# Kernel tuning notes

Hardware: AMD Instinct MI355X
Metric: run time of the kernel (lower is better)

Reference implementation:

```python
import jax, jax.numpy as jnp
import numpy as np
from jax import lax

PRE_NMS_TOPN = 6000
POST_NMS_TOPN = 300
NMS_IOU = 0.7
VARIANCES = np.array([0.1, 0.1, 0.2, 0.2], dtype=np.float32)


def setup_inputs() -> dict:
    key = jax.random.key(0)
    k1, k2, k3, k4 = jax.random.split(key, 4)
    B, FH, FW, K = 32, 128, 128, 9
    A = FH * FW * K  # 147456 total anchors
    rpn_bbox_deltas = jax.random.normal(k1, (B, A, 4), dtype=jnp.float32) * 0.1
    rpn_labels = jax.random.normal(k2, (B, FH, FW, K), dtype=jnp.float32)
    # Anchors in [y1, x1, y2, x2] with y1<y2, x1<x2 on a ~1024px image.
    ctr = jax.random.uniform(k3, (A, 2), dtype=jnp.float32) * 1024.0
    wh = jax.random.uniform(k4, (A, 2), dtype=jnp.float32) * 224.0 + 32.0
    anchors = jnp.concatenate([ctr - 0.5 * wh, ctr + 0.5 * wh], axis=-1)
    return {"rpn_bbox_deltas": rpn_bbox_deltas, "rpn_labels": rpn_labels, "anchors": anchors}


def get_bboxes_from_deltas(anchors, deltas):
    # anchors: [A, 4] (y1,x1,y2,x2); deltas: [B, A, 4] (dy,dx,dh,dw)
    anc_w = anchors[..., 3] - anchors[..., 1]
    anc_h = anchors[..., 2] - anchors[..., 0]
    anc_cx = anchors[..., 1] + 0.5 * anc_w
    anc_cy = anchors[..., 0] + 0.5 * anc_h
    bb_w = jnp.exp(deltas[..., 3]) * anc_w
    bb_h = jnp.exp(deltas[..., 2]) * anc_h
    bb_cx = deltas[..., 1] * anc_w + anc_cx
    bb_cy = deltas[..., 0] * anc_h + anc_cy
    y1 = bb_cy - 0.5 * bb_h
    x1 = bb_cx - 0.5 * bb_w
    y2 = bb_h + y1
    x2 = bb_w + x1
    return jnp.stack([y1, x1, y2, x2], axis=-1)


def nms_per_image(boxes, scores, iou_threshold, num_keep):
    # boxes: [N, 4] sorted by descending score; scores: [N]
    y1, x1, y2, x2 = boxes[:, 0], boxes[:, 1], boxes[:, 2], boxes[:, 3]
    areas = (y2 - y1) * (x2 - x1)

    def step(scores_rem, _):
        idx = jnp.argmax(scores_rem)
        valid = jnp.isfinite(scores_rem[idx])
        b = boxes[idx]
        iy1 = jnp.maximum(b[0], y1)
        ix1 = jnp.maximum(b[1], x1)
        iy2 = jnp.minimum(b[2], y2)
        ix2 = jnp.minimum(b[3], x2)
        inter = jnp.clip(iy2 - iy1, 0.0) * jnp.clip(ix2 - ix1, 0.0)
        b_area = (b[2] - b[0]) * (b[3] - b[1])
        iou = inter / (areas + b_area - inter + 1e-9)
        # IoU(box, itself) == 1 > threshold, so the picked box is also suppressed.
        new_scores = jnp.where(iou > iou_threshold, -jnp.inf, scores_rem)
        return new_scores, (idx, valid)

    _, (keep_idx, valid) = lax.scan(step, scores, None, length=num_keep)
    vf = valid.astype(boxes.dtype)
    keep_boxes = boxes[keep_idx] * vf[:, None]  # zero-pad invalid slots
    keep_scores = scores[keep_idx] * vf
    return keep_boxes, keep_scores


def reference(rpn_bbox_deltas, rpn_labels, anchors):
    A = anchors.shape[0]
    B = rpn_bbox_deltas.shape[0]
    deltas = rpn_bbox_deltas.reshape(B, A, 4) * jnp.asarray(VARIANCES)
    labels = jax.nn.softmax(rpn_labels, axis=-1).reshape(B, A)
    rpn_bboxes = get_bboxes_from_deltas(anchors, deltas)  # [B, A, 4]
    # top-k pre-NMS filter (lax.top_k output is already sorted descending)
    pre_scores, pre_idx = lax.top_k(labels, PRE_NMS_TOPN)  # [B, P]
    pre_boxes = jnp.take_along_axis(rpn_bboxes, pre_idx[..., None], axis=1)  # [B, P, 4]
    nms_fn = lambda b, s: nms_per_image(b, s, NMS_IOU, POST_NMS_TOPN)
    roi_bboxes, roi_scores = jax.vmap(nms_fn)(pre_boxes, pre_scores)
    return roi_bboxes, roi_scores
```

## Files before the change

### kernel.cpp

```cpp
#include <hip/hip_runtime.h>
#include <cstdint>
#include <cstddef>

#pragma clang fp contract(off)

#define KCLS 9
#define PRE_N 6000
#define POST_N 300
#define NMS_IOU_T 0.7f
#define HIST_BLOCK 256
#define CHUNKS_PER_IMG 32
#define NMS_BLOCK 512
#define PICK_BLOCK 256
#define NSEG 4
#define SEG_CAP 4096

__global__ void __launch_bounds__(256)
softmax_hist_kernel(const float* __restrict__ labels,
                    float* __restrict__ scores,
                    unsigned int* __restrict__ ghist,
                    int ngroups, int gpi) {
    __shared__ unsigned int h[2048];
    const int tid = threadIdx.x;
    for (int i = tid; i < 2048; i += 256) h[i] = 0u;
    __syncthreads();
    const int g = blockIdx.x * 256 + tid;
    if (g < ngroups) {
        const float* x = labels + (size_t)g * KCLS;
        float v[KCLS];
        float m = -1e30f;
        #pragma unroll
        for (int k = 0; k < KCLS; ++k) { v[k] = x[k]; m = fmaxf(m, v[k]); }
        float e[KCLS];
        float s = 0.f;
        #pragma unroll
        for (int k = 0; k < KCLS; ++k) { e[k] = expf(v[k] - m); s += e[k]; }
        float* o = scores + (size_t)g * KCLS;
        #pragma unroll
        for (int k = 0; k < KCLS; ++k) {
            float r = e[k] / s;
            o[k] = r;
            atomicAdd(&h[(__float_as_uint(r) >> 21) & 2047u], 1u);
        }
    }
    __syncthreads();
    const int img0 = (blockIdx.x * 256) / gpi;
    unsigned int* gh = ghist + (size_t)img0 * 2048;
    for (int i = tid; i < 2048; i += 256) {
        unsigned int c = h[i];
        if (c) atomicAdd(&gh[i], c);
    }
}

__global__ void hist_kernel(const float* __restrict__ scores,
                            unsigned int* __restrict__ ghist,
                            const unsigned int* __restrict__ state,
                            int A, int shift, int bins, unsigned int pmask) {
    __shared__ unsigned int h[2048];
    const int img = blockIdx.y;
    const int chunk = blockIdx.x;
    const int tid = threadIdx.x;
    for (int i = tid; i < bins; i += HIST_BLOCK) h[i] = 0u;
    __syncthreads();
    unsigned int prefix = pmask ? (state[img * 2 + 0] & pmask) : 0u;
    const int per = A / CHUNKS_PER_IMG;
    const float* sc = scores + (size_t)img * A + (size_t)chunk * per;
    for (int i = tid; i < per; i += HIST_BLOCK) {
        unsigned int v = __float_as_uint(sc[i]);
        if ((v & pmask) == prefix)
            atomicAdd(&h[(v >> shift) & (unsigned)(bins - 1)], 1u);
    }
    __syncthreads();
    unsigned int* gh = ghist + (size_t)img * 2048;
    for (int i = tid; i < bins; i += HIST_BLOCK) {
        unsigned int c = h[i];
        if (c) atomicAdd(&gh[i], c);
    }
}

__global__ void __launch_bounds__(PICK_BLOCK)
pick_kernel(const unsigned int* __restrict__ ghist,
            unsigned int* __restrict__ state,
            int shift, int bins, int first_pass) {
    const int img = blockIdx.x;
    const int t = threadIdx.x;
    const unsigned int* gh = ghist + (size_t)img * 2048;
    __shared__ unsigned int cnt[2048];
    __shared__ unsigned int ssum[PICK_BLOCK];
    const int per = bins / PICK_BLOCK;
    unsigned int my = 0;
    for (int i = 0; i < per; ++i) {
        unsigned int c = gh[t * per + i];
        cnt[t * per + i] = c;
        my += c;
    }
    ssum[t] = my;
    __syncthreads();
    for (int d = 1; d < PICK_BLOCK; d <<= 1) {
        unsigned int v = (t + d < PICK_BLOCK) ? ssum[t + d] : 0u;
        __syncthreads();
        ssum[t] += v;
        __syncthreads();
    }
    unsigned int prefix = first_pass ? 0u : state[img * 2 + 0];
    unsigned int krem = first_pass ? (unsigned)PRE_N : state[img * 2 + 1];
    unsigned int above = ssum[t] - my;
    if (above < krem && ssum[t] >= krem) {
        unsigned int cum = above;
        for (int b = per - 1; b >= 0; --b) {
            unsigned int c = cnt[t * per + b];
            if (cum + c >= krem) {
                state[img * 2 + 0] = prefix | ((unsigned int)(t * per + b) << shift);
                state[img * 2 + 1] = krem - cum;
                break;
            }
            cum += c;
        }
    }
}

#define CE(a, b, u) { if ((v[a] > v[b]) == (u)) { unsigned long long t_ = v[a]; v[a] = v[b]; v[b] = t_; } }
#define REG3(u) { CE(0,4,u) CE(1,5,u) CE(2,6,u) CE(3,7,u) \
                  CE(0,2,u) CE(1,3,u) CE(4,6,u) CE(5,7,u) \
                  CE(0,1,u) CE(2,3,u) CE(4,5,u) CE(6,7,u) }

__global__ void __launch_bounds__(512)
compact_sort_kernel(const float* __restrict__ scores,
                    const unsigned int* __restrict__ state,
                    unsigned long long* __restrict__ pool,
                    unsigned int* __restrict__ counts,
                    int A) {
    __shared__ unsigned long long lin[SEG_CAP];
    __shared__ unsigned int plo[2][SEG_CAP];
    __shared__ unsigned int phi[2][SEG_CAP];
    __shared__ unsigned int cnt;
    const int img = blockIdx.y;
    const int seg = blockIdx.x;
    const int tid = threadIdx.x;
    const int lane = tid & 63;
    const int w = tid >> 6;
    const float* sc = scores + (size_t)img * A;
    const unsigned int T = state[img * 2 + 0];

    if (tid == 0) cnt = 0u;
    for (int i = tid; i < SEG_CAP; i += 512) lin[i] = ~0ull;
    __syncthreads();

    const int ngr = A >> 6;
    const int nj = ngr / NSEG;
    for (int j = w; j < nj; j += 8) {
        int g = seg + j * NSEG;
        int i = (g << 6) + lane;
        unsigned int sv = __float_as_uint(sc[i]);
        bool push = (sv >= T);
        unsigned long long bal = __ballot(push ? 1 : 0);
        if (push) {
            int leader = __ffsll(bal) - 1;
            int rank = __popcll(bal & ((1ull << lane) - 1ull));
            unsigned int base = 0;
            if (lane == leader) base = atomicAdd(&cnt, (unsigned int)__popcll(bal));
            base = (unsigned int)__shfl((int)base, leader);
            unsigned int pos = base + (unsigned int)rank;
            if (pos < SEG_CAP)
                lin[pos] = (((unsigned long long)(~sv)) << 32) | (unsigned long long)(unsigned int)i;
        }
    }
    __syncthreads();

    int n = (int)cnt; if (n > SEG_CAP) n = SEG_CAP;
    int P2 = 512; while (P2 < n) P2 <<= 1;
    const int NT = P2 >> 3;
    const int t = tid;
    const bool act = (t < NT);

    unsigned long long v[8];
    if (act) {
        #pragma unroll
        for (int e = 0; e < 8; ++e) v[e] = lin[(t << 3) + e];
        CE(0,1,true) CE(2,3,false) CE(4,5,true) CE(6,7,false)
        CE(0,2,true) CE(1,3,true) CE(4,6,false) CE(5,7,false)
        CE(0,1,true) CE(2,3,true) CE(4,5,false) CE(6,7,false)
        bool u8 = ((t & 1) == 0);
        REG3(u8)
    }
    int b = 0;
    for (int k = 16; k <= P2; k <<= 1) {
        const bool up = (((t << 3) & k) == 0);
        for (int j = k >> 1; j >= 8; j >>= 1) {
            const int c = j >> 3;
            if (act) {
                #pragma unroll
                for (int e = 0; e < 8; ++e) {
                    int idx = e * NT + t;
                    plo[b][idx] = (unsigned int)v[e];
                    phi[b][idx] = (unsigned int)(v[e] >> 32);
                }
            }
            __syncthreads();
            if (act) {
                const int q = t ^ c;
                const bool keep_min = (up == ((t & c) == 0));
                #pragma unroll
                for (int e = 0; e < 8; ++e) {
                    int idx = e * NT + q;
                    unsigned long long wv = ((unsigned long long)phi[b][idx] << 32)
                                          | (unsigned long long)plo[b][idx];
                    bool less = v[e] < wv;
                    v[e] = (less == keep_min) ? v[e] : wv;
                }
            }
            b ^= 1;
        }
        if (act) { REG3(up) }
    }

    unsigned long long* gp = pool + ((size_t)img * NSEG + seg) * SEG_CAP;
    if (act) {
        #pragma unroll
        for (int e = 0; e < 8; ++e) {
            int r = (t << 3) + e;
            if (r < n) gp[r] = v[e];
        }
    }
    if (tid == 0) counts[img * NSEG + seg] = (unsigned int)n;
}

__global__ void __launch_bounds__(256)
rank_decode_kernel(const unsigned long long* __restrict__ pool,
                   const unsigned int* __restrict__ counts,
                   const float* __restrict__ deltas,
                   const float* __restrict__ anchors,
                   float* __restrict__ pre_boxes,
                   float* __restrict__ pre_scores,
                   int A) {
    __shared__ unsigned long long arr[2 * SEG_CAP];
    const int img = blockIdx.y;
    const int seg = blockIdx.x;
    const int tid = threadIdx.x;

    int c[NSEG], off[NSEG + 1];
    const unsigned long long* gp[NSEG];
    off[0] = 0;
    #pragma unroll
    for (int s = 0; s < NSEG; ++s) {
        int cs = (int)counts[img * NSEG + s];
        if (cs > SEG_CAP) cs = SEG_CAP;
        c[s] = cs;
        off[s + 1] = off[s] + cs;
        gp[s] = pool + ((size_t)img * NSEG + s) * SEG_CAP;
    }
    const int total = off[NSEG];
    const bool inlds = (total <= 2 * SEG_CAP);
    if (inlds) {
        #pragma unroll
        for (int s = 0; s < NSEG; ++s)
            for (int i = tid; i < c[s]; i += 256) arr[off[s] + i] = gp[s][i];
    }
    __syncthreads();

    const int m = c[seg];
    for (int i = tid; i < m; i += 256) {
        unsigned long long key = inlds ? arr[off[seg] + i] : gp[seg][i];
        int pos = i;
        #pragma unroll
        for (int s = 0; s < NSEG; ++s) {
            if (s == seg) continue;
            const unsigned long long* base = inlds ? (arr + off[s]) : gp[s];
            int lo = 0, hi = c[s];
            while (lo < hi) {
                int mid = (lo + hi) >> 1;
                if (base[mid] < key) lo = mid + 1; else hi = mid;
            }
            pos += lo;
        }
        if (pos < PRE_N) {
            unsigned int bidx = (unsigned int)(key & 0xFFFFFFFFull);
            unsigned int sbits = ~((unsigned int)(key >> 32));
            float score = __uint_as_float(sbits);
            float a0 = anchors[(size_t)bidx * 4 + 0];
            float a1 = anchors[(size_t)bidx * 4 + 1];
            float a2 = anchors[(size_t)bidx * 4 + 2];
            float a3 = anchors[(size_t)bidx * 4 + 3];
            const float* dd = deltas + ((size_t)img * A + bidx) * 4;
            float d0 = dd[0] * 0.1f;
            float d1 = dd[1] * 0.1f;
            float d2 = dd[2] * 0.2f;
            float d3 = dd[3] * 0.2f;
            float anc_w = a3 - a1;
            float anc_h = a2 - a0;
            float anc_cx = a1 + 0.5f * anc_w;
            float anc_cy = a0 + 0.5f * anc_h;
            float bb_w = expf(d3) * anc_w;
            float bb_h = expf(d2) * anc_h;
            float bb_cx = d1 * anc_w + anc_cx;
            float bb_cy = d0 * anc_h + anc_cy;
            float y1 = bb_cy - 0.5f * bb_h;
            float x1 = bb_cx - 0.5f * bb_w;
            float y2 = bb_h + y1;
            float x2 = bb_w + x1;
            float* ob = pre_boxes + ((size_t)img * PRE_N + pos) * 4;
            ob[0] = y1; ob[1] = x1; ob[2] = y2; ob[3] = x2;
            pre_scores[(size_t)img * PRE_N + pos] = score;
        }
    }
}

__global__ void __launch_bounds__(NMS_BLOCK)
nms_kernel(const float* __restrict__ pre_boxes,
           const float* __restrict__ pre_scores,
           float* __restrict__ out_boxes,
           float* __restrict__ out_scores) {
    const int img = blockIdx.x;
    const int tid = threadIdx.x;
    const int lane = tid & 63;
    const int grp = tid >> 6;
    const float4* bb4 = (const float4*)(pre_boxes + (size_t)img * PRE_N * 4);

    __shared__ float4 kept[POST_N];
    __shared__ float  kept_area[POST_N];
    __shared__ int    kept_idx[POST_N];
    __shared__ float4 chunkbox[64];
    __shared__ unsigned long long chunk_alive;
    __shared__ int kept_cnt;

    if (tid == 0) kept_cnt = 0;

    const int NCH = (PRE_N + 63) >> 6;

    float4 nb = make_float4(0.f, 0.f, 0.f, 0.f);
    if (grp == 0) nb = bb4[lane];

    for (int c = 0; c < NCH; ++c) {
        const int base = c << 6;
        if (grp == 0) chunkbox[lane] = nb;
        if (tid == 0) {
            int rem = PRE_N - base;
            chunk_alive = (rem >= 64) ? ~0ull : ((1ull << rem) - 1ull);
        }
        __syncthreads();

        if (grp == 0 && c + 1 < NCH) {
            int j = base + 64 + lane;
            nb = (j < PRE_N) ? bb4[j] : make_float4(0.f, 0.f, 0.f, 0.f);
        }

        const int K = kept_cnt;
        float4 mb = chunkbox[lane];
        float marea = (mb.z - mb.x) * (mb.w - mb.y);

        bool sup = false;
        for (int k = grp; k < K; k += 8) {
            float4 pb = kept[k];
            float pa = kept_area[k];
            float iy1 = fmaxf(pb.x, mb.x);
            float ix1 = fmaxf(pb.y, mb.y);
            float iy2 = fminf(pb.z, mb.z);
            float ix2 = fminf(pb.w, mb.w);
            float ih = iy2 - iy1; ih = ih > 0.f ? ih : 0.f;
            float iw = ix2 - ix1; iw = iw > 0.f ? iw : 0.f;
            float inter = ih * iw;
            float den = marea + pa - inter + 1e-9f;
            float hi = 0.7000007f * den;
            float lo = 0.6999993f * den;
            bool s = inter > hi;
            if (inter >= lo && inter <= hi)
                s = (inter / den) > NMS_IOU_T;
            if (s) { sup = true; break; }
        }
        unsigned long long bal = __ballot(sup ? 1 : 0);
        if (lane == 0 && bal) atomicAnd(&chunk_alive, ~bal);
        __syncthreads();

        if (grp == 0) {
            unsigned long long m = chunk_alive;
            int kc = K;
            while (m && kc < POST_N) {
                int i = __ffsll(m) - 1;
                float py1 = __shfl(mb.x, i);
                float px1 = __shfl(mb.y, i);
                float py2 = __shfl(mb.z, i);
                float px2 = __shfl(mb.w, i);
                float pa  = __shfl(marea, i);
                if (lane == i) {
                    kept[kc] = mb;
                    kept_area[kc] = marea;
                    kept_idx[kc] = base + i;
                }
                float iy1 = fmaxf(py1, mb.x);
                float ix1 = fmaxf(px1, mb.y);
                float iy2 = fminf(py2, mb.z);
                float ix2 = fminf(px2, mb.w);
                float ih = iy2 - iy1; ih = ih > 0.f ? ih : 0.f;
                float iw = ix2 - ix1; iw = iw > 0.f ? iw : 0.f;
                float inter = ih * iw;
                float den = marea + pa - inter + 1e-9f;
                float hi = 0.7000007f * den;
                float lo = 0.6999993f * den;
                bool s = inter > hi;
                if (inter >= lo && inter <= hi)
                    s = (inter / den) > NMS_IOU_T;
                unsigned long long sb = __ballot(s ? 1 : 0);
                m &= ~sb;
                m &= ~(1ull << i);
                ++kc;
            }
            if (lane == 0) kept_cnt = kc;
        }
        __syncthreads();
        if (kept_cnt >= POST_N) break;
    }

    const int kc = kept_cnt;
    for (int r = tid; r < kc; r += NMS_BLOCK) {
        float4 bx = kept[r];
        float* ob = out_boxes + ((size_t)img * POST_N + r) * 4;
        ob[0] = bx.x; ob[1] = bx.y; ob[2] = bx.z; ob[3] = bx.w;
        out_scores[(size_t)img * POST_N + r] =
            pre_scores[(size_t)img * PRE_N + kept_idx[r]];
    }
}

extern "C" void kernel_launch(void* const* d_in, const int* in_sizes, int n_in,
                              void* d_out, int out_size, void* d_ws, size_t ws_size,
                              hipStream_t stream) {
    const float* deltas  = (const float*)d_in[0];
    const float* labels  = (const float*)d_in[1];
    const float* anchors = (const float*)d_in[2];
    float* out = (float*)d_out;

    const int A = in_sizes[2] / 4;
    const int B = in_sizes[0] / (A * 4);
    const int ngroups = in_sizes[1] / KCLS;
    const int gpi = ngroups / B;

    float* scores     = (float*)d_ws;
    float* pre_boxes  = scores + (size_t)B * A;
    float* pre_scores = pre_boxes + (size_t)B * PRE_N * 4;
    unsigned int* hist  = (unsigned int*)(pre_scores + (size_t)B * PRE_N);
    unsigned int* state = hist + (size_t)3 * B * 2048;
    unsigned long long* pool = (unsigned long long*)(state + (size_t)B * 2);
    unsigned int* counts = (unsigned int*)(pool + (size_t)B * NSEG * SEG_CAP);

    float* out_boxes  = out;
    float* out_scores = out + (size_t)B * POST_N * 4;

    hipMemsetAsync(d_out, 0, (size_t)out_size * sizeof(float), stream);
    hipMemsetAsync(hist, 0, (size_t)3 * B * 2048 * sizeof(unsigned int), stream);

    softmax_hist_kernel<<<(ngroups + 255) / 256, 256, 0, stream>>>(
        labels, scores, hist + (size_t)0 * B * 2048, ngroups, gpi);
    pick_kernel<<<B, PICK_BLOCK, 0, stream>>>(hist + (size_t)0 * B * 2048, state, 21, 2048, 1);

    dim3 hgrid(CHUNKS_PER_IMG, B);
    hist_kernel<<<hgrid, HIST_BLOCK, 0, stream>>>(scores, hist + (size_t)1 * B * 2048, state, A, 10, 2048, 0xFFE00000u);
    pick_kernel<<<B, PICK_BLOCK, 0, stream>>>(hist + (size_t)1 * B * 2048, state, 10, 2048, 0);
    hist_kernel<<<hgrid, HIST_BLOCK, 0, stream>>>(scores, hist + (size_t)2 * B * 2048, state, A, 0, 1024, 0xFFFFFC00u);
    pick_kernel<<<B, PICK_BLOCK, 0, stream>>>(hist + (size_t)2 * B * 2048, state, 0, 1024, 0);

    dim3 sgrid(NSEG, B);
    compact_sort_kernel<<<sgrid, 512, 0, stream>>>(scores, state, pool, counts, A);
    rank_decode_kernel<<<sgrid, 256, 0, stream>>>(pool, counts, deltas, anchors,
                                                  pre_boxes, pre_scores, A);

    nms_kernel<<<B, NMS_BLOCK, 0, stream>>>(pre_boxes, pre_scores, out_boxes, out_scores);
}
```

Measured before the change: 304.2 us.

## Precompute intra-chunk IoU bitmask across all warps and resolve with serial scan

Within each 64-box chunk, the 8 wavefronts now compute the full 64x64 intra-chunk suppression matrix in parallel (8 rows each) into shared memory, OR-reduced into per-column masks. Wave 0 then resolves the greedy keep order with a cheap bitmask scan over supcol instead of a shuffle and IoU evaluation per kept box. This trades serial per-kept IoU/ballot latency for redundant parallel IoU work on every chunk, including chunks where few boxes survive.

```diff
diff --git a/kernel.cpp b/kernel.cpp
--- a/kernel.cpp
+++ b/kernel.cpp
@@ -14,6 +14,22 @@
 #define PICK_BLOCK 256
 #define NSEG 4
 #define SEG_CAP 4096
+
+#define SUPP(pb, pa, mbx, mar, out) \
+    bool out; { \
+        float iy1_ = fmaxf((pb).x, (mbx).x); \
+        float ix1_ = fmaxf((pb).y, (mbx).y); \
+        float iy2_ = fminf((pb).z, (mbx).z); \
+        float ix2_ = fminf((pb).w, (mbx).w); \
+        float ih_ = iy2_ - iy1_; ih_ = ih_ > 0.f ? ih_ : 0.f; \
+        float iw_ = ix2_ - ix1_; iw_ = iw_ > 0.f ? iw_ : 0.f; \
+        float inter_ = ih_ * iw_; \
+        float den_ = (mar) + (pa) - inter_ + 1e-9f; \
+        float hi_ = 0.7000007f * den_; \
+        float lo_ = 0.6999993f * den_; \
+        out = inter_ > hi_; \
+        if (inter_ >= lo_ && inter_ <= hi_) out = (inter_ / den_) > NMS_IOU_T; \
+    }
 
 __global__ void __launch_bounds__(256)
 softmax_hist_kernel(const float* __restrict__ labels,
@@ -320,6 +336,8 @@
     __shared__ float  kept_area[POST_N];
     __shared__ int    kept_idx[POST_N];
     __shared__ float4 chunkbox[64];
+    __shared__ unsigned long long part[8][64];
+    __shared__ unsigned long long supcol[64];
     __shared__ unsigned long long chunk_alive;
     __shared__ int kept_cnt;
 
@@ -352,57 +370,45 @@
         for (int k = grp; k < K; k += 8) {
             float4 pb = kept[k];
             float pa = kept_area[k];
-            float iy1 = fmaxf(pb.x, mb.x);
-            float ix1 = fmaxf(pb.y, mb.y);
-            float iy2 = fminf(pb.z, mb.z);
-            float ix2 = fminf(pb.w, mb.w);
-            float ih = iy2 - iy1; ih = ih > 0.f ? ih : 0.f;
-            float iw = ix2 - ix1; iw = iw > 0.f ? iw : 0.f;
-            float inter = ih * iw;
-            float den = marea + pa - inter + 1e-9f;
-            float hi = 0.7000007f * den;
-            float lo = 0.6999993f * den;
-            bool s = inter > hi;
-            if (inter >= lo && inter <= hi)
-                s = (inter / den) > NMS_IOU_T;
+            SUPP(pb, pa, mb, marea, s)
             if (s) { sup = true; break; }
         }
         unsigned long long bal = __ballot(sup ? 1 : 0);
         if (lane == 0 && bal) atomicAnd(&chunk_alive, ~bal);
+
+        unsigned long long pm = 0ull;
+        #pragma unroll
+        for (int u = 0; u < 8; ++u) {
+            const int i = (grp << 3) + u;
+            float4 pb = chunkbox[i];
+            float pa = (pb.z - pb.x) * (pb.w - pb.y);
+            SUPP(pb, pa, mb, marea, s)
+            if (s) pm |= (1ull << i);
+        }
+        part[grp][lane] = pm;
         __syncthreads();
 
         if (grp == 0) {
-            unsigned long long m = chunk_alive;
+            unsigned long long col = part[0][lane] | part[1][lane] | part[2][lane] | part[3][lane]
+                                   | part[4][lane] | part[5][lane] | part[6][lane] | part[7][lane];
+            supcol[lane] = col;
+            const unsigned long long extm = chunk_alive;
+            unsigned long long aliveset = 0ull;
             int kc = K;
-            while (m && kc < POST_N) {
-                int i = __ffsll(m) - 1;
-                float py1 = __shfl(mb.x, i);
-                float px1 = __shfl(mb.y, i);
-                float py2 = __shfl(mb.z, i);
-                float px2 = __shfl(mb.w, i);
-                float pa  = __shfl(marea, i);
-                if (lane == i) {
-                    kept[kc] = mb;
-                    kept_area[kc] = marea;
-                    kept_idx[kc] = base + i;
+            #pragma unroll 8
+            for (int i = 0; i < 64; ++i) {
+                unsigned long long mi = supcol[i];
+                bool keep = (((extm >> i) & 1ull) != 0ull) &&
+                            ((mi & aliveset) == 0ull) && (kc < POST_N);
+                if (keep) {
+                    if (lane == i) {
+                        kept[kc] = mb;
+                        kept_area[kc] = marea;
+                        kept_idx[kc] = base + i;
+                    }
+                    aliveset |= (1ull << i);
+                    ++kc;
                 }
-                float iy1 = fmaxf(py1, mb.x);
-                float ix1 = fmaxf(px1, mb.y);
-                float iy2 = fminf(py2, mb.z);
-                float ix2 = fminf(px2, mb.w);
-                float ih = iy2 - iy1; ih = ih > 0.f ? ih : 0.f;
-                float iw = ix2 - ix1; iw = iw > 0.f ? iw : 0.f;
-                float inter = ih * iw;
-                float den = marea + pa - inter + 1e-9f;
-                float hi = 0.7000007f * den;
-                float lo = 0.6999993f * den;
-                bool s = inter > hi;
-                if (inter >= lo && inter <= hi)
-                    s = (inter / den) > NMS_IOU_T;
-                unsigned long long sb = __ballot(s ? 1 : 0);
-                m &= ~sb;
-                m &= ~(1ull << i);
-                ++kc;
             }
             if (lane == 0) kept_cnt = kc;
         }
```

Result: faster. 289.5 us (-4.8%).
